# Optimization experiments

Hardware: AMD Instinct MI355X
Metric: run time of the kernel (lower is better)

## Reference

```python
import jax, jax.numpy as jnp
import numpy as np

B, C, H = 4, 512, 4096
IC = C // 2


def setup_inputs() -> dict:
    key = jax.random.key(0)
    ks = jax.random.split(key, 9)
    s = 0.02
    return {
        "x": jax.random.normal(ks[0], (B, C, H), dtype=jnp.float32),
        "w_phi": jax.random.normal(ks[1], (IC, C), dtype=jnp.float32) * s,
        "b_phi": jax.random.normal(ks[2], (IC,), dtype=jnp.float32) * s,
        "w_theta": jax.random.normal(ks[3], (IC, C), dtype=jnp.float32) * s,
        "b_theta": jax.random.normal(ks[4], (IC,), dtype=jnp.float32) * s,
        "w_g": jax.random.normal(ks[5], (IC, C), dtype=jnp.float32) * s,
        "b_g": jax.random.normal(ks[6], (IC,), dtype=jnp.float32) * s,
        "w_mask": jax.random.normal(ks[7], (C, IC), dtype=jnp.float32) * s,
        "b_mask": jax.random.normal(ks[8], (C,), dtype=jnp.float32) * s,
    }


def reference(x, w_phi, b_phi, w_theta, b_theta, w_g, b_g, w_mask, b_mask):
    # conv1d kernel_size=1 == channel matmul. x: [b, c, h]
    phi = jnp.einsum('ic,bch->bih', w_phi, x) + b_phi[None, :, None]      # [b, ic, h]
    theta = jnp.einsum('ic,bch->bhi', w_theta, x) + b_theta[None, None, :]  # [b, h, ic]
    g = jnp.einsum('ic,bch->bhi', w_g, x) + b_g[None, None, :]             # [b, h, ic]
    scores = jnp.einsum('bqi,bik->bqk', theta, phi)                        # [b, h, h]
    # torch Softmax(dim=1) on [b, h_q, h_k] normalizes over the QUERY axis (axis=1)
    attn = jax.nn.softmax(scores, axis=1)
    ag = jnp.einsum('bqk,bki->bqi', attn, g)                               # [b, h, ic]
    mask = jnp.einsum('ci,bhi->bch', w_mask, ag) + b_mask[None, :, None]   # [b, c, h]
    return mask + x
```

## Files before the change

kernel.cpp:

```cpp
#include <hip/hip_runtime.h>
#include <hip/hip_bf16.h>
#include <hip/hip_fp16.h>
#include <type_traits>

constexpr int BB = 4;
constexpr int CC = 512;
constexpr int HH = 4096;
constexpr int IC = 256;

typedef _Float16 f16x8v __attribute__((ext_vector_type(8)));
typedef __bf16   bf16x8v __attribute__((ext_vector_type(8)));
typedef float    f32x4v __attribute__((ext_vector_type(4)));

__device__ __forceinline__ void gll16(const void* g, void* l) {
  __builtin_amdgcn_global_load_lds(
      (const __attribute__((address_space(1))) unsigned int*)g,
      (__attribute__((address_space(3))) unsigned int*)l, 16, 0, 0);
}

__device__ __forceinline__ f32x4v mfma16(f16x8v a, f16x8v b, f32x4v c) {
  return __builtin_amdgcn_mfma_f32_16x16x32_f16(a, b, c, 0, 0, 0);
}
__device__ __forceinline__ f32x4v mfma16(bf16x8v a, bf16x8v b, f32x4v c) {
  return __builtin_amdgcn_mfma_f32_16x16x32_bf16(a, b, c, 0, 0, 0);
}

__device__ __forceinline__ unsigned short hbits(float f) {
  __half h = __float2half(f);
  unsigned short b; __builtin_memcpy(&b, &h, 2); return b;
}
__device__ __forceinline__ unsigned short bbits(float f) {
  __hip_bfloat16 h = __float2bfloat16(f);
  unsigned short b; __builtin_memcpy(&b, &h, 2); return b;
}

template <int MODE>
__launch_bounds__(256)
__global__ void mgemm128(const void* __restrict__ Aall, const void* __restrict__ Ball,
                         const void* __restrict__ Ball2,
                         void* __restrict__ outP, void* __restrict__ out2P,
                         const float* __restrict__ bias, const float* __restrict__ bias2,
                         const float* __restrict__ xres, float* __restrict__ Z,
                         int M, int N, int K,
                         size_t sAb, size_t sBb, size_t sOb) {
  using ET = typename std::conditional<MODE == 3, bf16x8v, f16x8v>::type;

  __shared__ __align__(16) unsigned short sA[128 * 32];
  __shared__ __align__(16) unsigned short sB[128 * 32];

  const int zz = blockIdx.z;
  int b, which;
  if constexpr (MODE == 0) { b = zz & (BB - 1); which = zz >> 2; }
  else { b = zz; which = 0; }

  const unsigned short* __restrict__ A = (const unsigned short*)Aall + (size_t)b * sAb;
  const unsigned short* __restrict__ Bm =
      (const unsigned short*)((MODE == 0 && which) ? Ball2 : Ball) + (size_t)b * sBb;
  const float* __restrict__ biasSel = (MODE == 0 && which) ? bias2 : bias;
  void* __restrict__ outSel = (MODE == 0 && which) ? out2P : outP;

  const int t = threadIdx.x;
  const int lane = t & 63;
  const int w = t >> 6;
  const int wm = (w >> 1) << 6;
  const int wn = (w & 1) << 6;
  const int mBase = blockIdx.y * 128;
  const int nBase = blockIdx.x * 128;

  const int fr = lane & 15;
  const int fo = (lane >> 4) << 3;

  f32x4v acc[4][4] = {};

  for (int k0 = 0; k0 < K; k0 += 32) {
#pragma unroll
    for (int p = 0; p < 2; ++p) {
      const int u = t + (p << 8);
      const int r = u >> 2;
      const int cs = (u & 3) << 3;
      gll16(A + (size_t)(mBase + r) * K + (k0 + cs), sA + u * 8);
      gll16(Bm + (size_t)(nBase + r) * K + (k0 + cs), sB + u * 8);
    }
    __syncthreads();
    ET af[4], bf[4];
#pragma unroll
    for (int i = 0; i < 4; ++i)
      af[i] = *(const ET*)(sA + ((wm + (i << 4) + fr) << 5) + fo);
#pragma unroll
    for (int j = 0; j < 4; ++j)
      bf[j] = *(const ET*)(sB + ((wn + (j << 4) + fr) << 5) + fo);
#pragma unroll
    for (int i = 0; i < 4; ++i)
#pragma unroll
      for (int j = 0; j < 4; ++j)
        acc[i][j] = mfma16(af[i], bf[j], acc[i][j]);
    __syncthreads();
  }

  const int row0 = (lane >> 4) << 2;
  const int col = lane & 15;

  if constexpr (MODE == 2) {
    __hip_bfloat16* __restrict__ outB = (__hip_bfloat16*)outP;
    float csum[4] = {0.f, 0.f, 0.f, 0.f};
#pragma unroll
    for (int i = 0; i < 4; ++i) {
      const int m0 = mBase + wm + (i << 4) + row0;
#pragma unroll
      for (int j = 0; j < 4; ++j) {
        const int n = nBase + wn + (j << 4) + col;
        __hip_bfloat16* dst = outB + (size_t)b * sOb + (size_t)m0 * N + n;
#pragma unroll
        for (int rg = 0; rg < 4; ++rg) {
          const float e = __expf(acc[i][j][rg]);
          dst[(size_t)rg * N] = __float2bfloat16(e);
          csum[j] += e;
        }
      }
    }
#pragma unroll
    for (int j = 0; j < 4; ++j) {
      float s = csum[j];
      s += __shfl_xor(s, 16, 64);
      s += __shfl_xor(s, 32, 64);
      if (lane < 16) {
        const int n = nBase + wn + (j << 4) + col;
        atomicAdd(&Z[(size_t)b * N + n], s);
      }
    }
  } else {
#pragma unroll
    for (int i = 0; i < 4; ++i) {
      const int m0 = mBase + wm + (i << 4) + row0;
#pragma unroll
      for (int j = 0; j < 4; ++j) {
        const int n = nBase + wn + (j << 4) + col;
#pragma unroll
        for (int rg = 0; rg < 4; ++rg) {
          const int m = m0 + rg;
          const float v = acc[i][j][rg];
          if constexpr (MODE == 0) {
            ((__half*)outSel)[(size_t)b * sOb + (size_t)m * N + n] =
                __float2half(v + biasSel[n]);
          } else if constexpr (MODE == 1) {
            ((__hip_bfloat16*)outP)[(size_t)b * sOb + (size_t)m * N + n] =
                __float2bfloat16(v + bias[m]);
          } else {
            const size_t o = (size_t)b * sOb + (size_t)m * N + n;
            ((float*)outP)[o] = v + bias[m] + xres[o];
          }
        }
      }
    }
  }
}

__launch_bounds__(256)
__global__ void mgemm_ag(const __hip_bfloat16* __restrict__ Gall,
                         const __hip_bfloat16* __restrict__ Eall,
                         unsigned short* __restrict__ P16) {
  constexpr int KC = 1024;
  __shared__ __align__(16) unsigned short sA[256 * 32];
  __shared__ __align__(16) unsigned short sB[64 * 32];

  const int b = blockIdx.z;
  const int kc = blockIdx.x;
  const int qBase = blockIdx.y * 64;
  const int k0base = kc * KC;

  const unsigned short* __restrict__ G =
      (const unsigned short*)Gall + (size_t)b * IC * HH;
  const unsigned short* __restrict__ E =
      (const unsigned short*)Eall + (size_t)b * HH * HH;

  const int t = threadIdx.x;
  const int lane = t & 63;
  const int w = t >> 6;
  const int fr = lane & 15;
  const int fo = (lane >> 4) << 3;

  f32x4v acc[4][4] = {};

  for (int kk = 0; kk < KC; kk += 32) {
    const int k0 = k0base + kk;
#pragma unroll
    for (int p = 0; p < 4; ++p) {
      const int u = t + (p << 8);
      const int r = u >> 2;
      const int cs = (u & 3) << 3;
      gll16(G + (size_t)r * HH + (k0 + cs), sA + u * 8);
    }
    {
      const int r = t >> 2;
      const int cs = (t & 3) << 3;
      gll16(E + (size_t)(qBase + r) * HH + (k0 + cs), sB + t * 8);
    }
    __syncthreads();
    bf16x8v af[4], bf[4];
#pragma unroll
    for (int i = 0; i < 4; ++i)
      af[i] = *(const bf16x8v*)(sA + (((w << 6) + (i << 4) + fr) << 5) + fo);
#pragma unroll
    for (int j = 0; j < 4; ++j)
      bf[j] = *(const bf16x8v*)(sB + (((j << 4) + fr) << 5) + fo);
#pragma unroll
    for (int i = 0; i < 4; ++i)
#pragma unroll
      for (int j = 0; j < 4; ++j)
        acc[i][j] = mfma16(af[i], bf[j], acc[i][j]);
    __syncthreads();
  }

  unsigned short* __restrict__ P =
      P16 + ((size_t)kc * BB + b) * HH * IC;
  const int quad = lane >> 4;
  const int col = lane & 15;
#pragma unroll
  for (int i = 0; i < 4; ++i) {
    const int ic0 = (w << 6) + (i << 4) + (quad << 2);
#pragma unroll
    for (int j = 0; j < 4; ++j) {
      const int q = qBase + (j << 4) + col;
      ushort4 s = {hbits(acc[i][j][0]), hbits(acc[i][j][1]),
                   hbits(acc[i][j][2]), hbits(acc[i][j][3])};
      *(ushort4*)(P + (size_t)q * IC + ic0) = s;
    }
  }
}

__launch_bounds__(256)
__global__ void cvt_ag(const unsigned short* __restrict__ P16,
                       __hip_bfloat16* __restrict__ agB) {
  constexpr size_t CH = (size_t)BB * HH * IC;
  const size_t tIdx = (size_t)blockIdx.x * 256 + threadIdx.x;
  const f16x8v v0 = ((const f16x8v*)(P16))[tIdx];
  const f16x8v v1 = ((const f16x8v*)(P16 + CH))[tIdx];
  const f16x8v v2 = ((const f16x8v*)(P16 + 2 * CH))[tIdx];
  const f16x8v v3 = ((const f16x8v*)(P16 + 3 * CH))[tIdx];
  unsigned short o[8];
#pragma unroll
  for (int k = 0; k < 8; ++k) {
    const float s = (float)v0[k] + (float)v1[k] + (float)v2[k] + (float)v3[k];
    o[k] = bbits(s);
  }
  uint4 pack;
  __builtin_memcpy(&pack, o, 16);
  ((uint4*)agB)[tIdx] = pack;
}

__launch_bounds__(256)
__global__ void xpose(const float* __restrict__ x, __half* __restrict__ xT) {
  __shared__ float tile[64][65];
  const int b = blockIdx.z;
  const int h0 = blockIdx.x * 64;
  const int c0 = blockIdx.y * 64;
  const int lane = threadIdx.x & 63;
  const int r0 = threadIdx.x >> 6;
  const float* xb = x + (size_t)b * CC * HH;
#pragma unroll
  for (int rr = 0; rr < 16; ++rr) {
    const int c = r0 * 16 + rr;
    tile[c][lane] = xb[(size_t)(c0 + c) * HH + h0 + lane];
  }
  __syncthreads();
  __half* ob = xT + (size_t)b * HH * CC;
#pragma unroll
  for (int rr = 0; rr < 16; ++rr) {
    const int hl = r0 * 16 + rr;
    ob[(size_t)(h0 + hl) * CC + c0 + lane] = __float2half(tile[lane][hl]);
  }
}

__global__ void convw(const float* __restrict__ s0, const float* __restrict__ s1,
                      const float* __restrict__ s2, const float* __restrict__ s3,
                      __half* __restrict__ d0, __half* __restrict__ d1,
                      __half* __restrict__ d2, __hip_bfloat16* __restrict__ d3) {
  const int which = blockIdx.y;
  const int i = (blockIdx.x * 256 + threadIdx.x) * 4;
  if (which < 3) {
    const float* s = which == 0 ? s0 : (which == 1 ? s1 : s2);
    __half* d = which == 0 ? d0 : (which == 1 ? d1 : d2);
    const float4 v = *(const float4*)(s + i);
    d[i] = __float2half(v.x); d[i + 1] = __float2half(v.y);
    d[i + 2] = __float2half(v.z); d[i + 3] = __float2half(v.w);
  } else {
    const float4 v = *(const float4*)(s3 + i);
    d3[i] = __float2bfloat16(v.x); d3[i + 1] = __float2bfloat16(v.y);
    d3[i + 2] = __float2bfloat16(v.z); d3[i + 3] = __float2bfloat16(v.w);
  }
}

__launch_bounds__(256)
__global__ void gscale(unsigned int* __restrict__ g, const float* __restrict__ Z) {
  const size_t tid = (size_t)blockIdx.x * 256 + threadIdx.x;
  const size_t e0 = tid * 8;
  const int b = (int)(e0 >> 20);
  const int h = (int)(e0 & (HH - 1));
  const float* Zp = Z + ((size_t)b << 12) + h;
  uint4 raw = ((const uint4*)g)[tid];
  unsigned short* u = (unsigned short*)&raw;
#pragma unroll
  for (int k = 0; k < 8; ++k) {
    const float f = __uint_as_float(((unsigned)u[k]) << 16) / Zp[k];
    u[k] = bbits(f);
  }
  ((uint4*)g)[tid] = raw;
}

extern "C" void kernel_launch(void* const* d_in, const int* in_sizes, int n_in,
                              void* d_out, int out_size, void* d_ws, size_t ws_size,
                              hipStream_t stream) {
  (void)in_sizes; (void)n_in; (void)out_size; (void)ws_size;

  const float* x       = (const float*)d_in[0];
  const float* w_phi   = (const float*)d_in[1];
  const float* b_phi   = (const float*)d_in[2];
  const float* w_theta = (const float*)d_in[3];
  const float* b_theta = (const float*)d_in[4];
  const float* w_g     = (const float*)d_in[5];
  const float* b_g     = (const float*)d_in[6];
  const float* w_mask  = (const float*)d_in[7];
  const float* b_mask  = (const float*)d_in[8];
  float* out = (float*)d_out;

  char* p = (char*)d_ws;
  __hip_bfloat16* E = (__hip_bfloat16*)p;           p += (size_t)BB * HH * HH * 2;
  __half* xT       = (__half*)p;                    p += (size_t)BB * HH * CC * 2;
  __half* thetaH   = (__half*)p;                    p += (size_t)BB * HH * IC * 2;
  __half* phiH     = (__half*)p;                    p += (size_t)BB * HH * IC * 2;
  __hip_bfloat16* gB  = (__hip_bfloat16*)p;         p += (size_t)BB * IC * HH * 2;
  __hip_bfloat16* agB = (__hip_bfloat16*)p;         p += (size_t)BB * HH * IC * 2;
  __half* wthH = (__half*)p;                        p += (size_t)IC * CC * 2;
  __half* wphH = (__half*)p;                        p += (size_t)IC * CC * 2;
  __half* wgH  = (__half*)p;                        p += (size_t)IC * CC * 2;
  __hip_bfloat16* wmB = (__hip_bfloat16*)p;         p += (size_t)CC * IC * 2;
  float* Z = (float*)p;                             p += (size_t)BB * HH * 4;
  unsigned short* P16 = (unsigned short*)xT;

  const dim3 blk(256);

  convw<<<dim3(128, 4), blk, 0, stream>>>(w_phi, w_theta, w_g, w_mask, wphH, wthH, wgH, wmB);
  xpose<<<dim3(HH / 64, CC / 64, BB), blk, 0, stream>>>(x, xT);

  mgemm128<0><<<dim3(IC / 128, HH / 128, BB * 2), blk, 0, stream>>>(
      xT, wthH, wphH, thetaH, phiH, b_theta, b_phi, nullptr, nullptr,
      HH, IC, CC, (size_t)HH * CC, 0, (size_t)HH * IC);

  mgemm128<1><<<dim3(HH / 128, IC / 128, BB), blk, 0, stream>>>(
      wgH, xT, nullptr, gB, nullptr, b_g, nullptr, nullptr, nullptr,
      IC, HH, CC, 0, (size_t)HH * CC, (size_t)IC * HH);

  hipMemsetAsync(Z, 0, (size_t)BB * HH * sizeof(float), stream);
  mgemm128<2><<<dim3(HH / 128, HH / 128, BB), blk, 0, stream>>>(
      thetaH, phiH, nullptr, E, nullptr, nullptr, nullptr, nullptr, Z,
      HH, HH, IC, (size_t)HH * IC, (size_t)HH * IC, (size_t)HH * HH);

  gscale<<<dim3((BB * IC * HH / 8) / 256), blk, 0, stream>>>((unsigned int*)gB, Z);

  mgemm_ag<<<dim3(4, HH / 64, BB), blk, 0, stream>>>(gB, E, P16);
  cvt_ag<<<dim3((BB * HH * IC / 8) / 256), blk, 0, stream>>>(P16, agB);

  mgemm128<3><<<dim3(HH / 128, CC / 128, BB), blk, 0, stream>>>(
      wmB, agB, nullptr, out, nullptr, b_mask, nullptr, x, nullptr,
      CC, HH, IC, 0, (size_t)HH * IC, (size_t)CC * HH);
}
```

Before: 292.7 us.

## Fuse score recompute with attention-weighted g; drop materialized exp matrix

Stops writing the B×H×H bf16 exp-score matrix. The score GEMM now only accumulates the column sums Z. A new fused kernel recomputes theta·phi scores per tile, exponentiates them in registers and multiplies directly with the pre-scaled g, writing two split-K partials. The final mask GEMM sums both partials while loading from LDS, which removes the separate conversion kernel. This trades the large HBM round-trip of the exp matrix for a second score computation and uncached global loads of phi and g in the fused kernel.

```diff
diff --git a/kernel.cpp b/kernel.cpp
--- a/kernel.cpp
+++ b/kernel.cpp
@@ -1,7 +1,6 @@
 #include <hip/hip_runtime.h>
 #include <hip/hip_bf16.h>
 #include <hip/hip_fp16.h>
-#include <type_traits>
 
 constexpr int BB = 4;
 constexpr int CC = 512;
@@ -40,11 +39,9 @@
                          const void* __restrict__ Ball2,
                          void* __restrict__ outP, void* __restrict__ out2P,
                          const float* __restrict__ bias, const float* __restrict__ bias2,
-                         const float* __restrict__ xres, float* __restrict__ Z,
+                         float* __restrict__ Z,
                          int M, int N, int K,
                          size_t sAb, size_t sBb, size_t sOb) {
-  using ET = typename std::conditional<MODE == 3, bf16x8v, f16x8v>::type;
-
   __shared__ __align__(16) unsigned short sA[128 * 32];
   __shared__ __align__(16) unsigned short sB[128 * 32];
 
@@ -82,13 +79,13 @@
       gll16(Bm + (size_t)(nBase + r) * K + (k0 + cs), sB + u * 8);
     }
     __syncthreads();
-    ET af[4], bf[4];
-#pragma unroll
-    for (int i = 0; i < 4; ++i)
-      af[i] = *(const ET*)(sA + ((wm + (i << 4) + fr) << 5) + fo);
+    f16x8v af[4], bf[4];
+#pragma unroll
+    for (int i = 0; i < 4; ++i)
+      af[i] = *(const f16x8v*)(sA + ((wm + (i << 4) + fr) << 5) + fo);
 #pragma unroll
     for (int j = 0; j < 4; ++j)
-      bf[j] = *(const ET*)(sB + ((wn + (j << 4) + fr) << 5) + fo);
+      bf[j] = *(const f16x8v*)(sB + ((wn + (j << 4) + fr) << 5) + fo);
 #pragma unroll
     for (int i = 0; i < 4; ++i)
 #pragma unroll
@@ -101,23 +98,14 @@
   const int col = lane & 15;
 
   if constexpr (MODE == 2) {
-    __hip_bfloat16* __restrict__ outB = (__hip_bfloat16*)outP;
     float csum[4] = {0.f, 0.f, 0.f, 0.f};
 #pragma unroll
-    for (int i = 0; i < 4; ++i) {
-      const int m0 = mBase + wm + (i << 4) + row0;
-#pragma unroll
-      for (int j = 0; j < 4; ++j) {
-        const int n = nBase + wn + (j << 4) + col;
-        __hip_bfloat16* dst = outB + (size_t)b * sOb + (size_t)m0 * N + n;
-#pragma unroll
-        for (int rg = 0; rg < 4; ++rg) {
-          const float e = __expf(acc[i][j][rg]);
-          dst[(size_t)rg * N] = __float2bfloat16(e);
-          csum[j] += e;
-        }
-      }
-    }
+    for (int i = 0; i < 4; ++i)
+#pragma unroll
+      for (int j = 0; j < 4; ++j)
+#pragma unroll
+        for (int rg = 0; rg < 4; ++rg)
+          csum[j] += __expf(acc[i][j][rg]);
 #pragma unroll
     for (int j = 0; j < 4; ++j) {
       float s = csum[j];
@@ -142,12 +130,9 @@
           if constexpr (MODE == 0) {
             ((__half*)outSel)[(size_t)b * sOb + (size_t)m * N + n] =
                 __float2half(v + biasSel[n]);
-          } else if constexpr (MODE == 1) {
+          } else {
             ((__hip_bfloat16*)outP)[(size_t)b * sOb + (size_t)m * N + n] =
                 __float2bfloat16(v + bias[m]);
-          } else {
-            const size_t o = (size_t)b * sOb + (size_t)m * N + n;
-            ((float*)outP)[o] = v + bias[m] + xres[o];
           }
         }
       }
@@ -156,53 +141,120 @@
 }
 
 __launch_bounds__(256)
-__global__ void mgemm_ag(const __hip_bfloat16* __restrict__ Gall,
-                         const __hip_bfloat16* __restrict__ Eall,
-                         unsigned short* __restrict__ P16) {
-  constexpr int KC = 1024;
-  __shared__ __align__(16) unsigned short sA[256 * 32];
-  __shared__ __align__(16) unsigned short sB[64 * 32];
-
+__global__ void fusedattn(const __half* __restrict__ thetaAll,
+                          const __half* __restrict__ phiAll,
+                          const __hip_bfloat16* __restrict__ gAll,
+                          unsigned short* __restrict__ P16) {
   const int b = blockIdx.z;
   const int kc = blockIdx.x;
-  const int qBase = blockIdx.y * 64;
-  const int k0base = kc * KC;
-
-  const unsigned short* __restrict__ G =
-      (const unsigned short*)Gall + (size_t)b * IC * HH;
-  const unsigned short* __restrict__ E =
-      (const unsigned short*)Eall + (size_t)b * HH * HH;
+  const int q16 = blockIdx.y * 64 + (threadIdx.x >> 6) * 16;
+  const int lane = threadIdx.x & 63;
+  const int l15 = lane & 15;
+  const int l4 = lane >> 4;
+
+  const unsigned short* __restrict__ th =
+      (const unsigned short*)thetaAll + (size_t)b * HH * IC;
+  const unsigned short* __restrict__ ph =
+      (const unsigned short*)phiAll + (size_t)b * HH * IC;
+  const unsigned short* __restrict__ gs =
+      (const unsigned short*)gAll + (size_t)b * IC * HH;
+
+  f16x8v thf[8];
+#pragma unroll
+  for (int c = 0; c < 8; ++c)
+    thf[c] = *(const f16x8v*)(th + (size_t)(q16 + l15) * IC + c * 32 + l4 * 8);
+
+  f32x4v acc[16] = {};
+
+  const int pr0 = ((l15 >> 2) << 3) + (l15 & 3);
+  const int kstart = kc * 2048;
+
+#pragma unroll 2
+  for (int kk = 0; kk < 2048; kk += 32) {
+    const int k0 = kstart + kk;
+    const unsigned short* phB0 = ph + (size_t)(k0 + pr0) * IC + l4 * 8;
+    const unsigned short* phB1 = phB0 + 4 * IC;
+    f32x4v s0 = {}, s1 = {};
+#pragma unroll
+    for (int c = 0; c < 8; ++c) {
+      const f16x8v a0 = *(const f16x8v*)(phB0 + c * 32);
+      const f16x8v a1 = *(const f16x8v*)(phB1 + c * 32);
+      s0 = mfma16(a0, thf[c], s0);
+      s1 = mfma16(a1, thf[c], s1);
+    }
+    bf16x8v pf;
+#pragma unroll
+    for (int r = 0; r < 4; ++r) {
+      pf[r]     = (__bf16)__expf(s0[r]);
+      pf[r + 4] = (__bf16)__expf(s1[r]);
+    }
+#pragma unroll
+    for (int it = 0; it < 16; ++it) {
+      const bf16x8v ga =
+          *(const bf16x8v*)(gs + (size_t)(it * 16 + l15) * HH + k0 + l4 * 8);
+      acc[it] = mfma16(ga, pf, acc[it]);
+    }
+  }
+
+  unsigned short* __restrict__ P =
+      P16 + ((size_t)kc * BB + b) * HH * IC + (size_t)(q16 + l15) * IC;
+#pragma unroll
+  for (int it = 0; it < 16; ++it) {
+    const int ic0 = it * 16 + (l4 << 2);
+    ushort4 s = {hbits(acc[it][0]), hbits(acc[it][1]),
+                 hbits(acc[it][2]), hbits(acc[it][3])};
+    *(ushort4*)(P + ic0) = s;
+  }
+}
+
+__launch_bounds__(256)
+__global__ void finalgemm(const __half* __restrict__ wm,
+                          const unsigned short* __restrict__ P16,
+                          const float* __restrict__ bias,
+                          const float* __restrict__ xres,
+                          float* __restrict__ out) {
+  __shared__ __align__(16) unsigned short sA[128 * 32];
+  __shared__ __align__(16) unsigned short sB0[128 * 32];
+  __shared__ __align__(16) unsigned short sB1[128 * 32];
+
+  const int b = blockIdx.z;
+  const unsigned short* __restrict__ A = (const unsigned short*)wm;
+  const unsigned short* __restrict__ B0 = P16 + (size_t)b * HH * IC;
+  const unsigned short* __restrict__ B1 = B0 + (size_t)BB * HH * IC;
 
   const int t = threadIdx.x;
   const int lane = t & 63;
   const int w = t >> 6;
+  const int wm_ = (w >> 1) << 6;
+  const int wn = (w & 1) << 6;
+  const int mBase = blockIdx.y * 128;
+  const int nBase = blockIdx.x * 128;
+
   const int fr = lane & 15;
   const int fo = (lane >> 4) << 3;
 
   f32x4v acc[4][4] = {};
 
-  for (int kk = 0; kk < KC; kk += 32) {
-    const int k0 = k0base + kk;
-#pragma unroll
-    for (int p = 0; p < 4; ++p) {
+  for (int k0 = 0; k0 < IC; k0 += 32) {
+#pragma unroll
+    for (int p = 0; p < 2; ++p) {
       const int u = t + (p << 8);
       const int r = u >> 2;
       const int cs = (u & 3) << 3;
-      gll16(G + (size_t)r * HH + (k0 + cs), sA + u * 8);
-    }
-    {
-      const int r = t >> 2;
-      const int cs = (t & 3) << 3;
-      gll16(E + (size_t)(qBase + r) * HH + (k0 + cs), sB + t * 8);
+      gll16(A + (size_t)(mBase + r) * IC + (k0 + cs), sA + u * 8);
+      gll16(B0 + (size_t)(nBase + r) * IC + (k0 + cs), sB0 + u * 8);
+      gll16(B1 + (size_t)(nBase + r) * IC + (k0 + cs), sB1 + u * 8);
     }
     __syncthreads();
-    bf16x8v af[4], bf[4];
-#pragma unroll
-    for (int i = 0; i < 4; ++i)
-      af[i] = *(const bf16x8v*)(sA + (((w << 6) + (i << 4) + fr) << 5) + fo);
-#pragma unroll
-    for (int j = 0; j < 4; ++j)
-      bf[j] = *(const bf16x8v*)(sB + (((j << 4) + fr) << 5) + fo);
+    f16x8v af[4], bf[4];
+#pragma unroll
+    for (int i = 0; i < 4; ++i)
+      af[i] = *(const f16x8v*)(sA + ((wm_ + (i << 4) + fr) << 5) + fo);
+#pragma unroll
+    for (int j = 0; j < 4; ++j) {
+      const int o = ((wn + (j << 4) + fr) << 5) + fo;
+      bf[j] = *(const f16x8v*)(sB0 + o) + *(const f16x8v*)(sB1 + o);
+    }
 #pragma unroll
     for (int i = 0; i < 4; ++i)
 #pragma unroll
@@ -211,41 +263,22 @@
     __syncthreads();
   }
 
-  unsigned short* __restrict__ P =
-      P16 + ((size_t)kc * BB + b) * HH * IC;
-  const int quad = lane >> 4;
+  const int row0 = (lane >> 4) << 2;
   const int col = lane & 15;
 #pragma unroll
   for (int i = 0; i < 4; ++i) {
-    const int ic0 = (w << 6) + (i << 4) + (quad << 2);
+    const int m0 = mBase + wm_ + (i << 4) + row0;
 #pragma unroll
     for (int j = 0; j < 4; ++j) {
-      const int q = qBase + (j << 4) + col;
-      ushort4 s = {hbits(acc[i][j][0]), hbits(acc[i][j][1]),
-                   hbits(acc[i][j][2]), hbits(acc[i][j][3])};
-      *(ushort4*)(P + (size_t)q * IC + ic0) = s;
-    }
-  }
-}
-
-__launch_bounds__(256)
-__global__ void cvt_ag(const unsigned short* __restrict__ P16,
-                       __hip_bfloat16* __restrict__ agB) {
-  constexpr size_t CH = (size_t)BB * HH * IC;
-  const size_t tIdx = (size_t)blockIdx.x * 256 + threadIdx.x;
-  const f16x8v v0 = ((const f16x8v*)(P16))[tIdx];
-  const f16x8v v1 = ((const f16x8v*)(P16 + CH))[tIdx];
-  const f16x8v v2 = ((const f16x8v*)(P16 + 2 * CH))[tIdx];
-  const f16x8v v3 = ((const f16x8v*)(P16 + 3 * CH))[tIdx];
-  unsigned short o[8];
-#pragma unroll
-  for (int k = 0; k < 8; ++k) {
-    const float s = (float)v0[k] + (float)v1[k] + (float)v2[k] + (float)v3[k];
-    o[k] = bbits(s);
-  }
-  uint4 pack;
-  __builtin_memcpy(&pack, o, 16);
-  ((uint4*)agB)[tIdx] = pack;
+      const int n = nBase + wn + (j << 4) + col;
+#pragma unroll
+      for (int rg = 0; rg < 4; ++rg) {
+        const int m = m0 + rg;
+        const size_t o = (size_t)b * CC * HH + (size_t)m * HH + n;
+        out[o] = acc[i][j][rg] + bias[m] + xres[o];
+      }
+    }
+  }
 }
 
 __launch_bounds__(256)
@@ -274,20 +307,14 @@
 __global__ void convw(const float* __restrict__ s0, const float* __restrict__ s1,
                       const float* __restrict__ s2, const float* __restrict__ s3,
                       __half* __restrict__ d0, __half* __restrict__ d1,
-                      __half* __restrict__ d2, __hip_bfloat16* __restrict__ d3) {
+                      __half* __restrict__ d2, __half* __restrict__ d3) {
   const int which = blockIdx.y;
   const int i = (blockIdx.x * 256 + threadIdx.x) * 4;
-  if (which < 3) {
-    const float* s = which == 0 ? s0 : (which == 1 ? s1 : s2);
-    __half* d = which == 0 ? d0 : (which == 1 ? d1 : d2);
-    const float4 v = *(const float4*)(s + i);
-    d[i] = __float2half(v.x); d[i + 1] = __float2half(v.y);
-    d[i + 2] = __float2half(v.z); d[i + 3] = __float2half(v.w);
-  } else {
-    const float4 v = *(const float4*)(s3 + i);
-    d3[i] = __float2bfloat16(v.x); d3[i + 1] = __float2bfloat16(v.y);
-    d3[i + 2] = __float2bfloat16(v.z); d3[i + 3] = __float2bfloat16(v.w);
-  }
+  const float* s = which == 0 ? s0 : (which == 1 ? s1 : (which == 2 ? s2 : s3));
+  __half* d = which == 0 ? d0 : (which == 1 ? d1 : (which == 2 ? d2 : d3));
+  const float4 v = *(const float4*)(s + i);
+  d[i] = __float2half(v.x); d[i + 1] = __float2half(v.y);
+  d[i + 2] = __float2half(v.z); d[i + 3] = __float2half(v.w);
 }
 
 __launch_bounds__(256)
@@ -324,43 +351,39 @@
   float* out = (float*)d_out;
 
   char* p = (char*)d_ws;
-  __hip_bfloat16* E = (__hip_bfloat16*)p;           p += (size_t)BB * HH * HH * 2;
   __half* xT       = (__half*)p;                    p += (size_t)BB * HH * CC * 2;
   __half* thetaH   = (__half*)p;                    p += (size_t)BB * HH * IC * 2;
   __half* phiH     = (__half*)p;                    p += (size_t)BB * HH * IC * 2;
-  __hip_bfloat16* gB  = (__hip_bfloat16*)p;         p += (size_t)BB * IC * HH * 2;
-  __hip_bfloat16* agB = (__hip_bfloat16*)p;         p += (size_t)BB * HH * IC * 2;
+  __hip_bfloat16* gB = (__hip_bfloat16*)p;          p += (size_t)BB * IC * HH * 2;
   __half* wthH = (__half*)p;                        p += (size_t)IC * CC * 2;
   __half* wphH = (__half*)p;                        p += (size_t)IC * CC * 2;
   __half* wgH  = (__half*)p;                        p += (size_t)IC * CC * 2;
-  __hip_bfloat16* wmB = (__hip_bfloat16*)p;         p += (size_t)CC * IC * 2;
+  __half* wmH  = (__half*)p;                        p += (size_t)CC * IC * 2;
   float* Z = (float*)p;                             p += (size_t)BB * HH * 4;
   unsigned short* P16 = (unsigned short*)xT;
 
   const dim3 blk(256);
 
-  convw<<<dim3(128, 4), blk, 0, stream>>>(w_phi, w_theta, w_g, w_mask, wphH, wthH, wgH, wmB);
+  convw<<<dim3(128, 4), blk, 0, stream>>>(w_phi, w_theta, w_g, w_mask, wphH, wthH, wgH, wmH);
   xpose<<<dim3(HH / 64, CC / 64, BB), blk, 0, stream>>>(x, xT);
 
   mgemm128<0><<<dim3(IC / 128, HH / 128, BB * 2), blk, 0, stream>>>(
-      xT, wthH, wphH, thetaH, phiH, b_theta, b_phi, nullptr, nullptr,
+      xT, wthH, wphH, thetaH, phiH, b_theta, b_phi, nullptr,
       HH, IC, CC, (size_t)HH * CC, 0, (size_t)HH * IC);
 
   mgemm128<1><<<dim3(HH / 128, IC / 128, BB), blk, 0, stream>>>(
-      wgH, xT, nullptr, gB, nullptr, b_g, nullptr, nullptr, nullptr,
+      wgH, xT, nullptr, gB, nullptr, b_g, nullptr, nullptr,
       IC, HH, CC, 0, (size_t)HH * CC, (size_t)IC * HH);
 
   hipMemsetAsync(Z, 0, (size_t)BB * HH * sizeof(float), stream);
   mgemm128<2><<<dim3(HH / 128, HH / 128, BB), blk, 0, stream>>>(
-      thetaH, phiH, nullptr, E, nullptr, nullptr, nullptr, nullptr, Z,
-      HH, HH, IC, (size_t)HH * IC, (size_t)HH * IC, (size_t)HH * HH);
+      thetaH, phiH, nullptr, nullptr, nullptr, nullptr, nullptr, Z,
+      HH, HH, IC, (size_t)HH * IC, (size_t)HH * IC, 0);
 
   gscale<<<dim3((BB * IC * HH / 8) / 256), blk, 0, stream>>>((unsigned int*)gB, Z);
 
-  mgemm_ag<<<dim3(4, HH / 64, BB), blk, 0, stream>>>(gB, E, P16);
-  cvt_ag<<<dim3((BB * HH * IC / 8) / 256), blk, 0, stream>>>(P16, agB);
-
-  mgemm128<3><<<dim3(HH / 128, CC / 128, BB), blk, 0, stream>>>(
-      wmB, agB, nullptr, out, nullptr, b_mask, nullptr, x, nullptr,
-      CC, HH, IC, 0, (size_t)HH * IC, (size_t)CC * HH);
-}
+  fusedattn<<<dim3(2, HH / 64, BB), blk, 0, stream>>>(thetaH, phiH, gB, P16);
+
+  finalgemm<<<dim3(HH / 128, CC / 128, BB), blk, 0, stream>>>(
+      wmH, P16, b_mask, x, out);
+}
```

Result: slower. 707.7 us (+141.8%).

## Store exp-scores in MFMA fragment-blocked layout and read directly into registers

Applied to the files above, without the earlier changes.

The scores kernel now computes phi·theta^T so the exponentiated scores can be written as packed 16-byte MFMA B-fragments in a blocked layout, replacing scattered 2-byte bf16 stores. The attention·g kernel then reads those fragments straight from global memory into registers with a one-step prefetch, skipping the LDS staging for E. It also uses larger 128-query tiles with 8x4 accumulators per wave and occupancy hint 2. The column-sum reduction now uses shuffles across rows. The cost is more register pressure and a layout that only this pair of kernels understands.

```diff
diff --git a/kernel.cpp b/kernel.cpp
--- a/kernel.cpp
+++ b/kernel.cpp
@@ -40,7 +40,7 @@
                          const void* __restrict__ Ball2,
                          void* __restrict__ outP, void* __restrict__ out2P,
                          const float* __restrict__ bias, const float* __restrict__ bias2,
-                         const float* __restrict__ xres, float* __restrict__ Z,
+                         const float* __restrict__ xres,
                          int M, int N, int K,
                          size_t sAb, size_t sBb, size_t sOb) {
   using ET = typename std::conditional<MODE == 3, bf16x8v, f16x8v>::type;
@@ -100,127 +100,206 @@
   const int row0 = (lane >> 4) << 2;
   const int col = lane & 15;
 
-  if constexpr (MODE == 2) {
-    __hip_bfloat16* __restrict__ outB = (__hip_bfloat16*)outP;
-    float csum[4] = {0.f, 0.f, 0.f, 0.f};
-#pragma unroll
-    for (int i = 0; i < 4; ++i) {
-      const int m0 = mBase + wm + (i << 4) + row0;
-#pragma unroll
-      for (int j = 0; j < 4; ++j) {
-        const int n = nBase + wn + (j << 4) + col;
-        __hip_bfloat16* dst = outB + (size_t)b * sOb + (size_t)m0 * N + n;
-#pragma unroll
-        for (int rg = 0; rg < 4; ++rg) {
-          const float e = __expf(acc[i][j][rg]);
-          dst[(size_t)rg * N] = __float2bfloat16(e);
-          csum[j] += e;
+#pragma unroll
+  for (int i = 0; i < 4; ++i) {
+    const int m0 = mBase + wm + (i << 4) + row0;
+#pragma unroll
+    for (int j = 0; j < 4; ++j) {
+      const int n = nBase + wn + (j << 4) + col;
+#pragma unroll
+      for (int rg = 0; rg < 4; ++rg) {
+        const int m = m0 + rg;
+        const float v = acc[i][j][rg];
+        if constexpr (MODE == 0) {
+          ((__half*)outSel)[(size_t)b * sOb + (size_t)m * N + n] =
+              __float2half(v + biasSel[n]);
+        } else if constexpr (MODE == 1) {
+          ((__hip_bfloat16*)outP)[(size_t)b * sOb + (size_t)m * N + n] =
+              __float2bfloat16(v + bias[m]);
+        } else {
+          const size_t o = (size_t)b * sOb + (size_t)m * N + n;
+          ((float*)outP)[o] = v + bias[m] + xres[o];
         }
       }
     }
-#pragma unroll
-    for (int j = 0; j < 4; ++j) {
-      float s = csum[j];
-      s += __shfl_xor(s, 16, 64);
-      s += __shfl_xor(s, 32, 64);
-      if (lane < 16) {
-        const int n = nBase + wn + (j << 4) + col;
-        atomicAdd(&Z[(size_t)b * N + n], s);
-      }
-    }
-  } else {
-#pragma unroll
-    for (int i = 0; i < 4; ++i) {
-      const int m0 = mBase + wm + (i << 4) + row0;
-#pragma unroll
-      for (int j = 0; j < 4; ++j) {
-        const int n = nBase + wn + (j << 4) + col;
-#pragma unroll
-        for (int rg = 0; rg < 4; ++rg) {
-          const int m = m0 + rg;
-          const float v = acc[i][j][rg];
-          if constexpr (MODE == 0) {
-            ((__half*)outSel)[(size_t)b * sOb + (size_t)m * N + n] =
-                __float2half(v + biasSel[n]);
-          } else if constexpr (MODE == 1) {
-            ((__hip_bfloat16*)outP)[(size_t)b * sOb + (size_t)m * N + n] =
-                __float2bfloat16(v + bias[m]);
-          } else {
-            const size_t o = (size_t)b * sOb + (size_t)m * N + n;
-            ((float*)outP)[o] = v + bias[m] + xres[o];
-          }
-        }
-      }
-    }
   }
 }
 
 __launch_bounds__(256)
-__global__ void mgemm_ag(const __hip_bfloat16* __restrict__ Gall,
-                         const __hip_bfloat16* __restrict__ Eall,
-                         unsigned short* __restrict__ P16) {
-  constexpr int KC = 1024;
-  __shared__ __align__(16) unsigned short sA[256 * 32];
-  __shared__ __align__(16) unsigned short sB[64 * 32];
+__global__ void scores_blk(const __half* __restrict__ thetaAll,
+                           const __half* __restrict__ phiAll,
+                           unsigned short* __restrict__ Eblk,
+                           float* __restrict__ Z) {
+  __shared__ __align__(16) unsigned short sA[128 * 32];
+  __shared__ __align__(16) unsigned short sB[128 * 32];
 
   const int b = blockIdx.z;
-  const int kc = blockIdx.x;
-  const int qBase = blockIdx.y * 64;
-  const int k0base = kc * KC;
-
-  const unsigned short* __restrict__ G =
-      (const unsigned short*)Gall + (size_t)b * IC * HH;
-  const unsigned short* __restrict__ E =
-      (const unsigned short*)Eall + (size_t)b * HH * HH;
+  const unsigned short* __restrict__ A =
+      (const unsigned short*)phiAll + (size_t)b * HH * IC;
+  const unsigned short* __restrict__ Bm =
+      (const unsigned short*)thetaAll + (size_t)b * HH * IC;
 
   const int t = threadIdx.x;
   const int lane = t & 63;
   const int w = t >> 6;
+  const int wk = (w >> 1) << 6;
+  const int wq = (w & 1) << 6;
+  const int kBase = blockIdx.y * 128;
+  const int qBase = blockIdx.x * 128;
+
   const int fr = lane & 15;
   const int fo = (lane >> 4) << 3;
-
-  f32x4v acc[4][4] = {};
+  const int pr0 = ((fr >> 2) << 3) + (fr & 3);
+
+  f32x4v a0[2][4] = {};
+  f32x4v a1[2][4] = {};
+
+  for (int k0 = 0; k0 < IC; k0 += 32) {
+#pragma unroll
+    for (int p = 0; p < 2; ++p) {
+      const int u = t + (p << 8);
+      const int r = u >> 2;
+      const int cs = (u & 3) << 3;
+      gll16(A + (size_t)(kBase + r) * IC + (k0 + cs), sA + u * 8);
+      gll16(Bm + (size_t)(qBase + r) * IC + (k0 + cs), sB + u * 8);
+    }
+    __syncthreads();
+    f16x8v af0[2], af1[2], bf[4];
+#pragma unroll
+    for (int ch = 0; ch < 2; ++ch) {
+      af0[ch] = *(const f16x8v*)(sA + ((wk + (ch << 5) + pr0) << 5) + fo);
+      af1[ch] = *(const f16x8v*)(sA + ((wk + (ch << 5) + pr0 + 4) << 5) + fo);
+    }
+#pragma unroll
+    for (int j = 0; j < 4; ++j)
+      bf[j] = *(const f16x8v*)(sB + ((wq + (j << 4) + fr) << 5) + fo);
+#pragma unroll
+    for (int ch = 0; ch < 2; ++ch)
+#pragma unroll
+      for (int j = 0; j < 4; ++j) {
+        a0[ch][j] = mfma16(af0[ch], bf[j], a0[ch][j]);
+        a1[ch][j] = mfma16(af1[ch], bf[j], a1[ch][j]);
+      }
+    __syncthreads();
+  }
+
+  const int quad = lane >> 4;
+  float csum[2][8];
+#pragma unroll
+  for (int ch = 0; ch < 2; ++ch)
+#pragma unroll
+    for (int s = 0; s < 8; ++s) csum[ch][s] = 0.f;
+
+#pragma unroll
+  for (int ch = 0; ch < 2; ++ch) {
+    const int k32 = (kBase + wk + (ch << 5)) >> 5;
+#pragma unroll
+    for (int j = 0; j < 4; ++j) {
+      float e[8];
+#pragma unroll
+      for (int r = 0; r < 4; ++r) {
+        e[r]     = __expf(a0[ch][j][r]);
+        e[r + 4] = __expf(a1[ch][j][r]);
+      }
+      bf16x8v pf;
+#pragma unroll
+      for (int s = 0; s < 8; ++s) {
+        pf[s] = (__bf16)e[s];
+        csum[ch][s] += e[s];
+      }
+      const int q16 = (qBase + wq + (j << 4)) >> 4;
+      uint4 bits;
+      __builtin_memcpy(&bits, &pf, 16);
+      *(uint4*)(Eblk + ((((size_t)b * 256 + q16) * 128 + k32) << 9) + lane * 8) = bits;
+    }
+  }
+#pragma unroll
+  for (int ch = 0; ch < 2; ++ch) {
+#pragma unroll
+    for (int s = 0; s < 8; ++s) {
+      float v = csum[ch][s];
+      v += __shfl_xor(v, 1, 64);
+      v += __shfl_xor(v, 2, 64);
+      v += __shfl_xor(v, 4, 64);
+      v += __shfl_xor(v, 8, 64);
+      if (fr == 0) {
+        const int key = kBase + wk + (ch << 5) + (quad << 3) + s;
+        atomicAdd(&Z[(size_t)b * HH + key], v);
+      }
+    }
+  }
+}
+
+__launch_bounds__(256, 2)
+__global__ void ag_blk(const __hip_bfloat16* __restrict__ Gall,
+                       const unsigned short* __restrict__ Eblk,
+                       unsigned short* __restrict__ P16) {
+  constexpr int KC = 1024;
+  __shared__ __align__(16) unsigned short sA[256 * 32];
+
+  const int b = blockIdx.z;
+  const int kc = blockIdx.x;
+  const int qBase = blockIdx.y * 128;
+  const int t = threadIdx.x;
+  const int lane = t & 63;
+  const int w = t >> 6;
+  const int wq = (w >> 1) << 6;
+  const int wic = (w & 1) << 7;
+  const int fr = lane & 15;
+  const int fo = (lane >> 4) << 3;
+  const int k0 = kc * KC;
+
+  const unsigned short* __restrict__ G =
+      (const unsigned short*)Gall + (size_t)b * IC * HH;
+  const unsigned short* __restrict__ EB =
+      Eblk + (((size_t)b * 256 + ((qBase + wq) >> 4)) << 16) + lane * 8;
+
+  f32x4v acc[8][4] = {};
+  bf16x8v bc[4], bn[4];
+
+  {
+    const int k32 = k0 >> 5;
+#pragma unroll
+    for (int j = 0; j < 4; ++j)
+      bc[j] = *(const bf16x8v*)(EB + (((size_t)j * 128 + k32) << 9));
+  }
 
   for (int kk = 0; kk < KC; kk += 32) {
-    const int k0 = k0base + kk;
 #pragma unroll
     for (int p = 0; p < 4; ++p) {
       const int u = t + (p << 8);
       const int r = u >> 2;
       const int cs = (u & 3) << 3;
-      gll16(G + (size_t)r * HH + (k0 + cs), sA + u * 8);
-    }
+      gll16(G + (size_t)r * HH + (k0 + kk + cs), sA + u * 8);
+    }
+    __syncthreads();
     {
-      const int r = t >> 2;
-      const int cs = (t & 3) << 3;
-      gll16(E + (size_t)(qBase + r) * HH + (k0 + cs), sB + t * 8);
-    }
-    __syncthreads();
-    bf16x8v af[4], bf[4];
-#pragma unroll
-    for (int i = 0; i < 4; ++i)
-      af[i] = *(const bf16x8v*)(sA + (((w << 6) + (i << 4) + fr) << 5) + fo);
-#pragma unroll
-    for (int j = 0; j < 4; ++j)
-      bf[j] = *(const bf16x8v*)(sB + (((j << 4) + fr) << 5) + fo);
-#pragma unroll
-    for (int i = 0; i < 4; ++i)
+      const int k32n = (k0 + kk + 32) >> 5;
 #pragma unroll
       for (int j = 0; j < 4; ++j)
-        acc[i][j] = mfma16(af[i], bf[j], acc[i][j]);
-    __syncthreads();
-  }
-
-  unsigned short* __restrict__ P =
-      P16 + ((size_t)kc * BB + b) * HH * IC;
+        bn[j] = *(const bf16x8v*)(EB + (((size_t)j * 128 + k32n) << 9));
+    }
+#pragma unroll
+    for (int i = 0; i < 8; ++i) {
+      const bf16x8v af =
+          *(const bf16x8v*)(sA + ((wic + (i << 4) + fr) << 5) + fo);
+#pragma unroll
+      for (int j = 0; j < 4; ++j)
+        acc[i][j] = mfma16(af, bc[j], acc[i][j]);
+    }
+    __syncthreads();
+#pragma unroll
+    for (int j = 0; j < 4; ++j) bc[j] = bn[j];
+  }
+
+  unsigned short* __restrict__ P = P16 + ((size_t)kc * BB + b) * HH * IC;
   const int quad = lane >> 4;
-  const int col = lane & 15;
-#pragma unroll
-  for (int i = 0; i < 4; ++i) {
-    const int ic0 = (w << 6) + (i << 4) + (quad << 2);
+#pragma unroll
+  for (int i = 0; i < 8; ++i) {
+    const int ic0 = wic + (i << 4) + (quad << 2);
 #pragma unroll
     for (int j = 0; j < 4; ++j) {
-      const int q = qBase + (j << 4) + col;
+      const int q = qBase + wq + (j << 4) + fr;
       ushort4 s = {hbits(acc[i][j][0]), hbits(acc[i][j][1]),
                    hbits(acc[i][j][2]), hbits(acc[i][j][3])};
       *(ushort4*)(P + (size_t)q * IC + ic0) = s;
@@ -324,7 +403,7 @@
   float* out = (float*)d_out;
 
   char* p = (char*)d_ws;
-  __hip_bfloat16* E = (__hip_bfloat16*)p;           p += (size_t)BB * HH * HH * 2;
+  unsigned short* Eblk = (unsigned short*)p;        p += (size_t)BB * HH * HH * 2;
   __half* xT       = (__half*)p;                    p += (size_t)BB * HH * CC * 2;
   __half* thetaH   = (__half*)p;                    p += (size_t)BB * HH * IC * 2;
   __half* phiH     = (__half*)p;                    p += (size_t)BB * HH * IC * 2;
@@ -343,24 +422,22 @@
   xpose<<<dim3(HH / 64, CC / 64, BB), blk, 0, stream>>>(x, xT);
 
   mgemm128<0><<<dim3(IC / 128, HH / 128, BB * 2), blk, 0, stream>>>(
-      xT, wthH, wphH, thetaH, phiH, b_theta, b_phi, nullptr, nullptr,
+      xT, wthH, wphH, thetaH, phiH, b_theta, b_phi, nullptr,
       HH, IC, CC, (size_t)HH * CC, 0, (size_t)HH * IC);
 
   mgemm128<1><<<dim3(HH / 128, IC / 128, BB), blk, 0, stream>>>(
-      wgH, xT, nullptr, gB, nullptr, b_g, nullptr, nullptr, nullptr,
+      wgH, xT, nullptr, gB, nullptr, b_g, nullptr, nullptr,
       IC, HH, CC, 0, (size_t)HH * CC, (size_t)IC * HH);
 
   hipMemsetAsync(Z, 0, (size_t)BB * HH * sizeof(float), stream);
-  mgemm128<2><<<dim3(HH / 128, HH / 128, BB), blk, 0, stream>>>(
-      thetaH, phiH, nullptr, E, nullptr, nullptr, nullptr, nullptr, Z,
-      HH, HH, IC, (size_t)HH * IC, (size_t)HH * IC, (size_t)HH * HH);
+  scores_blk<<<dim3(HH / 128, HH / 128, BB), blk, 0, stream>>>(thetaH, phiH, Eblk, Z);
 
   gscale<<<dim3((BB * IC * HH / 8) / 256), blk, 0, stream>>>((unsigned int*)gB, Z);
 
-  mgemm_ag<<<dim3(4, HH / 64, BB), blk, 0, stream>>>(gB, E, P16);
+  ag_blk<<<dim3(4, HH / 128, BB), blk, 0, stream>>>(gB, Eblk, P16);
   cvt_ag<<<dim3((BB * HH * IC / 8) / 256), blk, 0, stream>>>(P16, agB);
 
   mgemm128<3><<<dim3(HH / 128, CC / 128, BB), blk, 0, stream>>>(
-      wmB, agB, nullptr, out, nullptr, b_mask, nullptr, x, nullptr,
+      wmB, agB, nullptr, out, nullptr, b_mask, nullptr, x,
       CC, HH, IC, 0, (size_t)HH * IC, (size_t)CC * HH);
 }
```

After: 315.0 us. 7.6% more time.
